# Optimization experiments

Hardware: AMD Instinct MI355X
Metric: run time of the kernel (lower is better)

## Reference

```python
import jax, jax.numpy as jnp
import numpy as np

N_NODES = 100000
N_EDGES = 600000
D = 128
N_CLASSES = 16


def _degrees(idx, n):
    ones = jnp.ones(idx.shape[0], dtype=jnp.float32)
    return jax.ops.segment_sum(ones, idx, num_segments=n)


def graph_conv(src, dst, h, W, b):
    # DGL GraphConv, norm='both': D_out^{-1/2} A D_in^{-1/2} h W + b
    n = h.shape[0]
    deg_out = jnp.maximum(_degrees(src, n), 1.0)
    deg_in = jnp.maximum(_degrees(dst, n), 1.0)
    h = h * jax.lax.rsqrt(deg_out)[:, None]          # src-side norm
    h = h @ W                                         # dense transform
    msg = h[src]                                      # gather  [E, d]
    agg = jax.ops.segment_sum(msg, dst, num_segments=n)  # scatter-add
    agg = agg * jax.lax.rsqrt(deg_in)[:, None]        # dst-side norm
    return agg + b


def setup_inputs() -> dict:
    key = jax.random.key(0)
    ks = jax.random.split(key, 8)
    h = jax.random.normal(ks[0], (N_NODES, D), dtype=jnp.float32)
    src = jax.random.randint(ks[1], (N_EDGES,), 0, N_NODES)
    dst = jax.random.randint(ks[2], (N_EDGES,), 0, N_NODES)
    s = 1.0 / np.sqrt(D)
    W1 = jax.random.normal(ks[3], (D, D), dtype=jnp.float32) * s
    b1 = jnp.zeros((D,), dtype=jnp.float32)
    W2 = jax.random.normal(ks[4], (D, D), dtype=jnp.float32) * s
    b2 = jnp.zeros((D,), dtype=jnp.float32)
    Wc = jax.random.normal(ks[5], (D, N_CLASSES), dtype=jnp.float32) * s
    bc = jnp.zeros((N_CLASSES,), dtype=jnp.float32)
    return {"h": h, "src": src, "dst": dst, "W1": W1, "b1": b1,
            "W2": W2, "b2": b2, "Wc": Wc, "bc": bc}


def reference(h, src, dst, W1, b1, W2, b2, Wc, bc):
    h = jax.nn.relu(graph_conv(src, dst, h, W1, b1))
    h = jax.nn.relu(graph_conv(src, dst, h, W2, b2))
    return h @ Wc + bc
```

## Files before the change

kernel.cpp:

```cpp
#include <hip/hip_runtime.h>


typedef __attribute__((ext_vector_type(4))) _Float16 half4_t;
typedef __attribute__((ext_vector_type(16))) float floatx16;

__global__ __launch_bounds__(256) void scan1_kernel(
    const int* __restrict__ cntI, const int* __restrict__ cntO,
    int* __restrict__ excl, int* __restrict__ bsum,
    float* __restrict__ rs_out, float* __restrict__ rs_in, int n)
{
    __shared__ int tmp[256];
    int i = blockIdx.x * 256 + threadIdx.x;
    int v = 0;
    if (i < n) {
        v = cntI[i];
        rs_in[i]  = rsqrtf(fmaxf((float)v, 1.0f));
        rs_out[i] = rsqrtf(fmaxf((float)cntO[i], 1.0f));
    }
    tmp[threadIdx.x] = v;
    __syncthreads();
    for (int off = 1; off < 256; off <<= 1) {
        int t = (threadIdx.x >= off) ? tmp[threadIdx.x - off] : 0;
        __syncthreads();
        tmp[threadIdx.x] += t;
        __syncthreads();
    }
    if (i < n) excl[i] = tmp[threadIdx.x] - v;
    if (threadIdx.x == 255) bsum[blockIdx.x] = tmp[255];
}

__global__ __launch_bounds__(1024) void scan2_kernel(int* __restrict__ bsum, int nb)
{
    __shared__ int tmp[1024];
    int t = threadIdx.x;
    int v = (t < nb) ? bsum[t] : 0;
    tmp[t] = v;
    __syncthreads();
    for (int off = 1; off < 1024; off <<= 1) {
        int x = (t >= off) ? tmp[t - off] : 0;
        __syncthreads();
        tmp[t] += x;
        __syncthreads();
    }
    if (t < nb) bsum[t] = tmp[t] - v;
}

__global__ __launch_bounds__(256) void scan3_kernel(
    int* __restrict__ excl, const int* __restrict__ bsum, int n)
{
    int i = blockIdx.x * 256 + threadIdx.x;
    if (i < n) excl[i] += bsum[blockIdx.x];
}

__global__ __launch_bounds__(256) void fill_kernel(
    const int* __restrict__ src, const int* __restrict__ dst,
    const int* __restrict__ rank, const int* __restrict__ starts,
    int* __restrict__ eidx, int E)
{
    int e = blockIdx.x * blockDim.x + threadIdx.x;
    if (e < E) {
        eidx[starts[dst[e]] + rank[e]] = src[e];
    }
}

__global__ __launch_bounds__(256) void wpack_kernel(
    const float* __restrict__ W1, const float* __restrict__ W2,
    _Float16* __restrict__ WB1, _Float16* __restrict__ WB2)
{
    int gid = blockIdx.x * 256 + threadIdx.x;
    int j = gid & 16383;
    int i   = j & 3;
    int col = (j >> 2) & 127;
    int g   = (j >> 9) & 1;
    int kt  = j >> 10;
    int k = kt * 8 + g * 4 + i;
    if (gid < 16384) WB1[j] = (_Float16)W1[k * 128 + col];
    else             WB2[j] = (_Float16)W2[k * 128 + col];
}

template <int MODE>
__device__ __forceinline__ void gemm_tile64(
    int bid, const void* __restrict__ Xv, const _Float16* __restrict__ WB,
    _Float16* __restrict__ T, int n)
{
    __shared__ _Float16 xa[64 * 128];
    char* xab = (char*)xa;

    const int tid  = threadIdx.x;
    const int lane = tid & 63;
    const int wv   = tid >> 6;
    const int m    = lane & 31;
    const int g    = lane >> 5;
    const int rhalf = wv & 1;
    const int chalf = wv >> 1;
    const int rbase = bid * 64 + rhalf * 32;

    {
        const int C = (tid & 31) * 4;
        const int rsub = tid >> 5;
#pragma unroll
        for (int p = 0; p < 8; ++p) {
            int R = p * 8 + rsub;
            int row = bid * 64 + R;
            half4_t a;
            if (row < n) {
                if (MODE == 0) {
                    const float* X = (const float*)Xv;
                    float4 v = *(const float4*)&X[(size_t)row * 128 + C];
                    a[0] = (_Float16)v.x;
                    a[1] = (_Float16)v.y;
                    a[2] = (_Float16)v.z;
                    a[3] = (_Float16)v.w;
                } else {
                    const _Float16* X = (const _Float16*)Xv;
                    a = *(const half4_t*)&X[(size_t)row * 128 + C];
                }
            } else {
                a[0] = a[1] = a[2] = a[3] = (_Float16)0.f;
            }
            int byte = (R * 256 + C * 2) ^ ((R & 7) << 4);
            *(half4_t*)(xab + byte) = a;
        }
    }
    __syncthreads();

    floatx16 acc0 = {}, acc1 = {};
    const int arow = rhalf * 32 + m;
    const _Float16* wb = WB + (size_t)(g * 128 + chalf * 64 + m) * 4;

#pragma unroll 2
    for (int kt = 0; kt < 16; ++kt) {
        int cbyte = kt * 16 + g * 8;
        half4_t a = *(const half4_t*)(xab + ((arow * 256 + cbyte) ^ ((m & 7) << 4)));
        const _Float16* wk = wb + (size_t)kt * 1024;
        half4_t b0 = *(const half4_t*)(wk);
        half4_t b1 = *(const half4_t*)(wk + 128);
        acc0 = __builtin_amdgcn_mfma_f32_32x32x8f16(a, b0, acc0, 0, 0, 0);
        acc1 = __builtin_amdgcn_mfma_f32_32x32x8f16(a, b1, acc1, 0, 0, 0);
    }

#pragma unroll
    for (int rg = 0; rg < 16; ++rg) {
        int rd = (rg & 3) + 8 * (rg >> 2) + 4 * g;
        int orow = rbase + rd;
        if (orow < n) {
            _Float16* tp = T + (size_t)orow * 128 + chalf * 64 + m;
            tp[0]  = (_Float16)acc0[rg];
            tp[32] = (_Float16)acc1[rg];
        }
    }
}

__global__ __launch_bounds__(256) void fused1_kernel(
    const float* __restrict__ h, const _Float16* __restrict__ WB1,
    _Float16* __restrict__ T1,
    const int* __restrict__ src, const int* __restrict__ dst,
    int* __restrict__ cntO, int* __restrict__ cntI, int* __restrict__ rank,
    int n, int E, int GB, int S)
{
    int bid = blockIdx.x;
    int g = bid / S, r = bid - g * S;
    if (r == 0 && g < GB) {
        gemm_tile64<0>(g, h, WB1, T1, n);
    } else {
        int ng = g + (r ? 1 : 0);
        if (ng > GB) ng = GB;
        int cb = bid - ng;
        int t = cb * 256 + threadIdx.x;
        if (t < E) {
            atomicAdd(&cntO[src[t]], 1);
        } else if (t < 2 * E) {
            int e = t - E;
            rank[e] = atomicAdd(&cntI[dst[e]], 1);
        }
    }
}

__global__ __launch_bounds__(256) void gemm2_kernel(
    const _Float16* __restrict__ X, const _Float16* __restrict__ WB,
    _Float16* __restrict__ T, int n)
{
    gemm_tile64<1>(blockIdx.x, X, WB, T, n);
}

template <int PES>
__device__ __forceinline__ void edge_accum(
    const _Float16* __restrict__ T, const int* __restrict__ eidx,
    const float* __restrict__ rs_out, int s0, int s1, int t, float acc[4])
{
    int j = s0;
    for (; j + 3 < s1; j += 4) {
        int4 s4 = *(const int4*)&eidx[j];
        half4_t va = *(const half4_t*)&T[(size_t)s4.x * 128 + t * 4];
        half4_t vb = *(const half4_t*)&T[(size_t)s4.y * 128 + t * 4];
        half4_t vc = *(const half4_t*)&T[(size_t)s4.z * 128 + t * 4];
        half4_t vd = *(const half4_t*)&T[(size_t)s4.w * 128 + t * 4];
        if (PES) {
            float ra = rs_out[s4.x], rb = rs_out[s4.y];
            float rc = rs_out[s4.z], rd = rs_out[s4.w];
#pragma unroll
            for (int i = 0; i < 4; ++i) {
                acc[i] = fmaf((float)va[i], ra, acc[i]);
                acc[i] = fmaf((float)vb[i], rb, acc[i]);
                acc[i] = fmaf((float)vc[i], rc, acc[i]);
                acc[i] = fmaf((float)vd[i], rd, acc[i]);
            }
        } else {
#pragma unroll
            for (int i = 0; i < 4; ++i)
                acc[i] += ((float)va[i] + (float)vb[i]) + ((float)vc[i] + (float)vd[i]);
        }
    }
    for (; j < s1; ++j) {
        int sA = eidx[j];
        half4_t va = *(const half4_t*)&T[(size_t)sA * 128 + t * 4];
        float ra = PES ? rs_out[sA] : 1.0f;
#pragma unroll
        for (int i = 0; i < 4; ++i) acc[i] = fmaf((float)va[i], ra, acc[i]);
    }
}

template <int PES, int NS>
__global__ __launch_bounds__(256) void gather_f16(
    const _Float16* __restrict__ T, const int* __restrict__ eidx,
    const int* __restrict__ starts, const float* __restrict__ rs_in,
    const float* __restrict__ rs_out, const float* __restrict__ bias,
    _Float16* __restrict__ Xout, int n, int E)
{
    int wave = (blockIdx.x * 256 + threadIdx.x) >> 6;
    int lane = threadIdx.x & 63;
    int q = lane >> 5;
    int t = lane & 31;
    int node = wave * 2 + q;
    if (node >= n) return;
    int s0 = starts[node];
    int s1 = (node + 1 < n) ? starts[node + 1] : E;

    float acc[4] = {0.f, 0.f, 0.f, 0.f};
    edge_accum<PES>(T, eidx, rs_out, s0, s1, t, acc);

    float ri = rs_in[node];
    float ro = NS ? rs_out[node] : 1.0f;
    float4 bv = *(const float4*)&bias[t * 4];
    float bb[4] = {bv.x, bv.y, bv.z, bv.w};
    half4_t o;
#pragma unroll
    for (int i = 0; i < 4; ++i) {
        float x = fmaxf(fmaf(acc[i], ri, bb[i]), 0.f) * ro;
        o[i] = (_Float16)x;
    }
    *(half4_t*)&Xout[(size_t)node * 128 + t * 4] = o;
}

__global__ __launch_bounds__(256) void classifier_kernel(
    const _Float16* __restrict__ X, const float* __restrict__ Wc,
    const float* __restrict__ bout, float* __restrict__ out, int n)
{
    __shared__ float wl[128 * 16];
    __shared__ _Float16 xs[16][128];
    const int tid = threadIdx.x;
    const int row0 = blockIdx.x * 16;
#pragma unroll
    for (int i0 = 0; i0 < 2; ++i0) {
        int i = tid + i0 * 256;
        ((float4*)wl)[i] = ((const float4*)Wc)[i];
    }
    {
        int r = tid >> 4, c8 = (tid & 15) * 8;
        int row = row0 + r;
        float4 v = make_float4(0.f, 0.f, 0.f, 0.f);
        if (row < n) v = *(const float4*)&X[(size_t)row * 128 + c8];
        *(float4*)&xs[r][c8] = v;
    }
    __syncthreads();
    int c = tid & 15, r = tid >> 4;
    float acc = 0.f;
#pragma unroll 4
    for (int k = 0; k < 128; k += 2) {
        float x0 = (float)xs[r][k];
        float x1 = (float)xs[r][k + 1];
        acc = fmaf(x0, wl[k * 16 + c], acc);
        acc = fmaf(x1, wl[(k + 1) * 16 + c], acc);
    }
    int row = row0 + r;
    if (row < n) out[(size_t)row * 16 + c] = acc + bout[c];
}

extern "C" void kernel_launch(void* const* d_in, const int* in_sizes, int n_in,
                              void* d_out, int out_size, void* d_ws, size_t ws_size,
                              hipStream_t stream)
{
    const float* h   = (const float*)d_in[0];
    const int*   src = (const int*)d_in[1];
    const int*   dst = (const int*)d_in[2];
    const float* W1  = (const float*)d_in[3];
    const float* b1  = (const float*)d_in[4];
    const float* W2  = (const float*)d_in[5];
    const float* b2  = (const float*)d_in[6];
    const float* Wc  = (const float*)d_in[7];
    const float* bc  = (const float*)d_in[8];
    float* out = (float*)d_out;

    const int n = in_sizes[0] / 128;
    const int E = in_sizes[1];
    const int nb = (n + 255) / 256;

    char* ws = (char*)d_ws;
    int*   cntO    = (int*)ws;
    int*   cntI    = cntO + n;
    int*   rank    = cntI + n;
    float* rs_out  = (float*)(rank + E);
    float* rs_in   = rs_out + n;
    int*   starts  = (int*)(rs_in + n);
    int*   bsum    = starts + n;
    int*   eidx    = bsum + 1024;
    _Float16* WB1  = (_Float16*)(eidx + E);
    _Float16* WB2  = WB1 + 16384;
    size_t off = ((size_t)((char*)(WB2 + 16384) - ws) + 255) & ~(size_t)255;
    _Float16* bufA = (_Float16*)(ws + off);
    _Float16* bufB = bufA + (size_t)n * 128;

    const int CB = (2 * E + 255) / 256;
    const int GB = (n + 63) / 64;
    const int S  = (CB + GB) / GB;

    hipMemsetAsync(cntO, 0, (size_t)2 * n * sizeof(int), stream);
    wpack_kernel<<<128, 256, 0, stream>>>(W1, W2, WB1, WB2);
    fused1_kernel<<<CB + GB, 256, 0, stream>>>(h, WB1, bufA, src, dst,
                                               cntO, cntI, rank, n, E, GB, S);
    scan1_kernel<<<nb, 256, 0, stream>>>(cntI, cntO, starts, bsum, rs_out, rs_in, n);
    scan2_kernel<<<1, 1024, 0, stream>>>(bsum, nb);
    scan3_kernel<<<nb, 256, 0, stream>>>(starts, bsum, n);
    fill_kernel<<<(E + 255) / 256, 256, 0, stream>>>(src, dst, rank, starts, eidx, E);

    int ablocks = (n + 7) / 8;

    gather_f16<1, 1><<<ablocks, 256, 0, stream>>>(bufA, eidx, starts, rs_in, rs_out, b1, bufB, n, E);

    gemm2_kernel<<<GB, 256, 0, stream>>>(bufB, WB2, bufA, n);

    gather_f16<0, 0><<<ablocks, 256, 0, stream>>>(bufA, eidx, starts, rs_in, rs_out, b2, bufB, n, E);

    classifier_kernel<<<(n + 15) / 16, 256, 0, stream>>>(bufB, Wc, bc, out, n);
}
```

Measured before the change: 191.1 us.

## Store feature matrices in 16-column panels so gathers stay cache-local

Feature buffers switch from row-major [n,128] to eight column panels of [n,16] f16. GEMM stores, the gather kernels and the classifier load all use the new layout. The gather now runs one panel per block group (4 lanes per node), so each pass over random source rows touches a 3.2MB panel that may fit in L2/LDS-adjacent cache instead of the full 25.6MB matrix. In exchange, edge indices and starts are re-read eight times, each random read becomes only 32 bytes, and the GEMM epilogue stores are strided.

After: 235.0 us. 1.23x slower.

```diff
diff --git a/kernel.cpp b/kernel.cpp
--- a/kernel.cpp
+++ b/kernel.cpp
@@ -113,7 +113,7 @@
                     a[3] = (_Float16)v.w;
                 } else {
                     const _Float16* X = (const _Float16*)Xv;
-                    a = *(const half4_t*)&X[(size_t)row * 128 + C];
+                    a = *(const half4_t*)&X[((size_t)(C >> 4) * n + row) * 16 + (C & 15)];
                 }
             } else {
                 a[0] = a[1] = a[2] = a[3] = (_Float16)0.f;
@@ -139,14 +139,17 @@
         acc1 = __builtin_amdgcn_mfma_f32_32x32x8f16(a, b1, acc1, 0, 0, 0);
     }
 
+    const int col0 = chalf * 64 + m;
+    const int col1 = col0 + 32;
+    _Float16* base0 = T + (size_t)(col0 >> 4) * n * 16 + (col0 & 15);
+    _Float16* base1 = T + (size_t)(col1 >> 4) * n * 16 + (col1 & 15);
 #pragma unroll
     for (int rg = 0; rg < 16; ++rg) {
         int rd = (rg & 3) + 8 * (rg >> 2) + 4 * g;
         int orow = rbase + rd;
         if (orow < n) {
-            _Float16* tp = T + (size_t)orow * 128 + chalf * 64 + m;
-            tp[0]  = (_Float16)acc0[rg];
-            tp[32] = (_Float16)acc1[rg];
+            base0[(size_t)orow * 16] = (_Float16)acc0[rg];
+            base1[(size_t)orow * 16] = (_Float16)acc1[rg];
         }
     }
 }
@@ -183,18 +186,32 @@
     gemm_tile64<1>(blockIdx.x, X, WB, T, n);
 }
 
-template <int PES>
-__device__ __forceinline__ void edge_accum(
+template <int PES, int NS>
+__global__ __launch_bounds__(256) void gather_panel(
     const _Float16* __restrict__ T, const int* __restrict__ eidx,
-    const float* __restrict__ rs_out, int s0, int s1, int t, float acc[4])
-{
+    const int* __restrict__ starts, const float* __restrict__ rs_in,
+    const float* __restrict__ rs_out, const float* __restrict__ bias,
+    _Float16* __restrict__ Xout, int n, int E, int BPP)
+{
+    int p  = blockIdx.x / BPP;
+    int nb = blockIdx.x - p * BPP;
+    int lane = threadIdx.x & 63;
+    int wv   = threadIdx.x >> 6;
+    int node = nb * 64 + wv * 16 + (lane >> 2);
+    int t    = lane & 3;
+    if (node >= n) return;
+    int s0 = starts[node];
+    int s1 = (node + 1 < n) ? starts[node + 1] : E;
+    const _Float16* Tp = T + (size_t)p * n * 16 + t * 4;
+
+    float acc[4] = {0.f, 0.f, 0.f, 0.f};
     int j = s0;
     for (; j + 3 < s1; j += 4) {
         int4 s4 = *(const int4*)&eidx[j];
-        half4_t va = *(const half4_t*)&T[(size_t)s4.x * 128 + t * 4];
-        half4_t vb = *(const half4_t*)&T[(size_t)s4.y * 128 + t * 4];
-        half4_t vc = *(const half4_t*)&T[(size_t)s4.z * 128 + t * 4];
-        half4_t vd = *(const half4_t*)&T[(size_t)s4.w * 128 + t * 4];
+        half4_t va = *(const half4_t*)&Tp[(size_t)s4.x * 16];
+        half4_t vb = *(const half4_t*)&Tp[(size_t)s4.y * 16];
+        half4_t vc = *(const half4_t*)&Tp[(size_t)s4.z * 16];
+        half4_t vd = *(const half4_t*)&Tp[(size_t)s4.w * 16];
         if (PES) {
             float ra = rs_out[s4.x], rb = rs_out[s4.y];
             float rc = rs_out[s4.z], rd = rs_out[s4.w];
@@ -213,35 +230,16 @@
     }
     for (; j < s1; ++j) {
         int sA = eidx[j];
-        half4_t va = *(const half4_t*)&T[(size_t)sA * 128 + t * 4];
+        half4_t va = *(const half4_t*)&Tp[(size_t)sA * 16];
         float ra = PES ? rs_out[sA] : 1.0f;
 #pragma unroll
         for (int i = 0; i < 4; ++i) acc[i] = fmaf((float)va[i], ra, acc[i]);
     }
-}
-
-template <int PES, int NS>
-__global__ __launch_bounds__(256) void gather_f16(
-    const _Float16* __restrict__ T, const int* __restrict__ eidx,
-    const int* __restrict__ starts, const float* __restrict__ rs_in,
-    const float* __restrict__ rs_out, const float* __restrict__ bias,
-    _Float16* __restrict__ Xout, int n, int E)
-{
-    int wave = (blockIdx.x * 256 + threadIdx.x) >> 6;
-    int lane = threadIdx.x & 63;
-    int q = lane >> 5;
-    int t = lane & 31;
-    int node = wave * 2 + q;
-    if (node >= n) return;
-    int s0 = starts[node];
-    int s1 = (node + 1 < n) ? starts[node + 1] : E;
-
-    float acc[4] = {0.f, 0.f, 0.f, 0.f};
-    edge_accum<PES>(T, eidx, rs_out, s0, s1, t, acc);
 
     float ri = rs_in[node];
     float ro = NS ? rs_out[node] : 1.0f;
-    float4 bv = *(const float4*)&bias[t * 4];
+    int cbase = p * 16 + t * 4;
+    float4 bv = *(const float4*)&bias[cbase];
     float bb[4] = {bv.x, bv.y, bv.z, bv.w};
     half4_t o;
 #pragma unroll
@@ -249,7 +247,7 @@
         float x = fmaxf(fmaf(acc[i], ri, bb[i]), 0.f) * ro;
         o[i] = (_Float16)x;
     }
-    *(half4_t*)&Xout[(size_t)node * 128 + t * 4] = o;
+    *(half4_t*)&Xout[((size_t)p * n + node) * 16 + t * 4] = o;
 }
 
 __global__ __launch_bounds__(256) void classifier_kernel(
@@ -269,7 +267,8 @@
         int r = tid >> 4, c8 = (tid & 15) * 8;
         int row = row0 + r;
         float4 v = make_float4(0.f, 0.f, 0.f, 0.f);
-        if (row < n) v = *(const float4*)&X[(size_t)row * 128 + c8];
+        if (row < n)
+            v = *(const float4*)&X[((size_t)(c8 >> 4) * n + row) * 16 + (c8 & 15)];
         *(float4*)&xs[r][c8] = v;
     }
     __syncthreads();
@@ -323,6 +322,7 @@
     const int CB = (2 * E + 255) / 256;
     const int GB = (n + 63) / 64;
     const int S  = (CB + GB) / GB;
+    const int BPP = (n + 63) / 64;
 
     hipMemsetAsync(cntO, 0, (size_t)2 * n * sizeof(int), stream);
     wpack_kernel<<<128, 256, 0, stream>>>(W1, W2, WB1, WB2);
@@ -333,13 +333,11 @@
     scan3_kernel<<<nb, 256, 0, stream>>>(starts, bsum, n);
     fill_kernel<<<(E + 255) / 256, 256, 0, stream>>>(src, dst, rank, starts, eidx, E);
 
-    int ablocks = (n + 7) / 8;
-
-    gather_f16<1, 1><<<ablocks, 256, 0, stream>>>(bufA, eidx, starts, rs_in, rs_out, b1, bufB, n, E);
+    gather_panel<1, 1><<<8 * BPP, 256, 0, stream>>>(bufA, eidx, starts, rs_in, rs_out, b1, bufB, n, E, BPP);
 
     gemm2_kernel<<<GB, 256, 0, stream>>>(bufB, WB2, bufA, n);
 
-    gather_f16<0, 0><<<ablocks, 256, 0, stream>>>(bufA, eidx, starts, rs_in, rs_out, b2, bufB, n, E);
+    gather_panel<0, 0><<<8 * BPP, 256, 0, stream>>>(bufA, eidx, starts, rs_in, rs_out, b2, bufB, n, E, BPP);
 
     classifier_kernel<<<(n + 15) / 16, 256, 0, stream>>>(bufB, Wc, bc, out, n);
 }
```
